# Kernel optimization log

Measured on AMD Instinct MI355X. Metric: run time of the kernel, lower is better.

Reference implementation:

```python
import jax, jax.numpy as jnp
import numpy as np

N = 100000   # nodes
E = 1600000  # edges (avg degree 16)
F_IN = 128
H = 128
C = 16


def setup_inputs() -> dict:
    key = jax.random.key(0)
    ks = jax.random.split(key, 13)
    s = 1.0 / np.sqrt(H)
    return {
        "x": jax.random.normal(ks[0], (N, F_IN), jnp.float32),
        "edge_index": jax.random.randint(ks[1], (2, E), 0, N, jnp.int32),
        "edge_weight": jax.random.uniform(ks[2], (E,), jnp.float32),
        "W1": jax.random.normal(ks[3], (F_IN, H), jnp.float32) * s,
        "b1": jnp.zeros((H,), jnp.float32),
        "W2": jax.random.normal(ks[4], (H, H), jnp.float32) * s,
        "b2": jnp.zeros((H,), jnp.float32),
        "Wg": jax.random.normal(ks[5], (H, H), jnp.float32) * s,
        "att_src": jax.random.normal(ks[6], (H,), jnp.float32) * s,
        "att_dst": jax.random.normal(ks[7], (H,), jnp.float32) * s,
        "bg": jnp.zeros((H,), jnp.float32),
        "Wc": jax.random.normal(ks[8], (H, C), jnp.float32) * s,
        "bc": jnp.zeros((C,), jnp.float32),
    }


def reference(x, edge_index, edge_weight, W1, b1, W2, b2, Wg, att_src, att_dst, bg, Wc, bc):
    n = x.shape[0]
    loop = jnp.arange(n, dtype=edge_index.dtype)
    src = jnp.concatenate([edge_index[0], loop])   # self loops (PyG default)
    dst = jnp.concatenate([edge_index[1], loop])
    ew = jnp.concatenate([edge_weight, jnp.ones((n,), x.dtype)])  # loop weight 1

    # GCN normalization: D^{-1/2} A D^{-1/2}, degree on dst with edge weights
    deg = jax.ops.segment_sum(ew, dst, num_segments=n)
    dinv = jnp.where(deg > 0, jax.lax.rsqrt(deg), 0.0)
    norm = dinv[src] * ew * dinv[dst]              # [E+N]

    def gcn(h, W, b):
        h = h @ W                                   # [N,H]
        agg = jax.ops.segment_sum(h[src] * norm[:, None], dst, num_segments=n)
        return agg + b

    h = jax.nn.relu(gcn(x, W1, b1))
    h = jax.nn.relu(gcn(h, W2, b2))                 # dropout inert in eval

    # GATConv, heads=1
    g = h @ Wg                                      # [N,H]
    a = jax.nn.leaky_relu((g @ att_src)[src] + (g @ att_dst)[dst], 0.2)
    amax = jax.ops.segment_max(a, dst, num_segments=n)
    ex = jnp.exp(a - amax[dst])
    denom = jax.ops.segment_sum(ex, dst, num_segments=n)
    alpha = ex / denom[dst]                         # edge softmax per dst
    out = jax.ops.segment_sum(g[src] * alpha[:, None], dst, num_segments=n) + bg
    out = jax.nn.relu(out)
    return out @ Wc + bc
```

## Files before the change

### kernel.cpp

```cpp
#include <hip/hip_runtime.h>
#include <hip/hip_fp16.h>

#define FIN 128
#define HD 128
#define COUT 16

#define SLOT_CAP 48
#define CS_BLOCKS 512
#define CB_SHIFT 9
#define CB_SIZE 512
#define CAP_B 10240
#define GMK_CELLS 64

typedef _Float16 half8 __attribute__((ext_vector_type(8)));
typedef float floatx4 __attribute__((ext_vector_type(4)));

__device__ __forceinline__ float lrelu02(float x) { return x > 0.f ? x : 0.2f * x; }

union U4H8 { uint4 q; __half2 h2[4]; };
union UQH8 { uint4 q; half8 h; _Float16 e[8]; };

__device__ __forceinline__ void h8f(const uint4 q, float* f) {
    U4H8 u; u.q = q;
    float2 a0 = __half22float2(u.h2[0]);
    float2 a1 = __half22float2(u.h2[1]);
    float2 a2 = __half22float2(u.h2[2]);
    float2 a3 = __half22float2(u.h2[3]);
    f[0] = a0.x; f[1] = a0.y; f[2] = a1.x; f[3] = a1.y;
    f[4] = a2.x; f[5] = a2.y; f[6] = a3.x; f[7] = a3.y;
}

__device__ __forceinline__ unsigned fkey(float f) {
    unsigned u = __float_as_uint(f);
    return (u & 0x80000000u) ? ~u : (u | 0x80000000u);
}
__device__ __forceinline__ float funkey(unsigned k) {
    return (k & 0x80000000u) ? __uint_as_float(k ^ 0x80000000u)
                             : __uint_as_float(~k);
}

__global__ void k_setup(const float* __restrict__ W1, const float* __restrict__ W2,
                        const float* __restrict__ Wg, __half* __restrict__ w1z,
                        __half* __restrict__ w2z, __half* __restrict__ wgz,
                        int* __restrict__ cur, unsigned* __restrict__ gmk) {
    int b = blockIdx.x;
    if (b < 24) {
        const float* W = (b < 8) ? W1 : (b < 16) ? W2 : Wg;
        __half* outp   = (b < 8) ? w1z : (b < 16) ? w2z : wgz;
        int t = (b & 7) * 256 + threadIdx.x;
        int lane = t & 63;
        int kc = (t >> 6) & 3;
        int nt = t >> 8;
        int kbase = kc * 32 + (lane >> 4) * 8;
        int col = nt * 16 + (lane & 15);
        UQH8 u;
#pragma unroll
        for (int j = 0; j < 8; j++)
            u.e[j] = (_Float16)W[(kbase + j) * 128 + col];
        ((uint4*)outp)[t] = u.q;
    } else {
        cur[threadIdx.x] = 0;
        for (int i = threadIdx.x; i < GMK_CELLS * 16; i += 256)
            gmk[i] = 0u;
    }
}

__device__ __forceinline__
void gemm_body_f32(int blk, const float* __restrict__ A, const __half* __restrict__ Wz,
                   __half* __restrict__ Out, int n) {
    int wave = threadIdx.x >> 6;
    int lane = threadIdx.x & 63;
    int m0 = blk * 64 + wave * 16;
    if (m0 >= n) return;
    int m = lane & 15;
    int quad = lane >> 4;

    half8 a[4];
#pragma unroll
    for (int kc = 0; kc < 4; kc++) {
        const float* p = &A[(size_t)(m0 + m) * 128 + kc * 32 + quad * 8];
        float4 f0 = *(const float4*)p;
        float4 f1 = *(const float4*)(p + 4);
        UQH8 u;
        u.e[0] = (_Float16)f0.x; u.e[1] = (_Float16)f0.y;
        u.e[2] = (_Float16)f0.z; u.e[3] = (_Float16)f0.w;
        u.e[4] = (_Float16)f1.x; u.e[5] = (_Float16)f1.y;
        u.e[6] = (_Float16)f1.z; u.e[7] = (_Float16)f1.w;
        a[kc] = u.h;
    }

    floatx4 acc[8];
#pragma unroll
    for (int nt = 0; nt < 8; nt++) acc[nt] = (floatx4){0.f, 0.f, 0.f, 0.f};

    const uint4* Wv = (const uint4*)Wz;
#pragma unroll
    for (int kc = 0; kc < 4; kc++) {
#pragma unroll
        for (int nt = 0; nt < 8; nt++) {
            UQH8 u;
            u.q = Wv[(nt * 4 + kc) * 64 + lane];
            acc[nt] = __builtin_amdgcn_mfma_f32_16x16x32_f16(a[kc], u.h, acc[nt], 0, 0, 0);
        }
    }
#pragma unroll
    for (int nt = 0; nt < 8; nt++) {
#pragma unroll
        for (int reg = 0; reg < 4; reg++) {
            Out[(size_t)(m0 + quad * 4 + reg) * 128 + nt * 16 + m] =
                __float2half(acc[nt][reg]);
        }
    }
}

__launch_bounds__(256)
__global__ void k_csc_gemm(const int* __restrict__ src, const int* __restrict__ dst,
                           const float* __restrict__ ew, int* __restrict__ cur,
                           int2* __restrict__ coarseBuf, int e,
                           const float* __restrict__ x, const __half* __restrict__ w1z,
                           __half* __restrict__ buf0, int n) {
    __shared__ int lcnt[256], lbase[256], lpos[256];
    if ((int)blockIdx.x < CS_BLOCKS) {
        int tid = threadIdx.x;
        lcnt[tid] = 0; lpos[tid] = 0;
        __syncthreads();
        int chunk = (e + CS_BLOCKS - 1) / CS_BLOCKS;
        int s0 = blockIdx.x * chunk;
        int s1 = min(s0 + chunk, e);
        for (int i = s0 + tid; i < s1; i += 256)
            atomicAdd(&lcnt[dst[i] >> CB_SHIFT], 1);
        __syncthreads();
        if (lcnt[tid] > 0) lbase[tid] = atomicAdd(&cur[tid], lcnt[tid]);
        __syncthreads();
        for (int i = s0 + tid; i < s1; i += 256) {
            int d = dst[i];
            int b = d >> CB_SHIFT;
            int pos = lbase[b] + atomicAdd(&lpos[b], 1);
            if (pos < CAP_B)
                coarseBuf[(size_t)b * CAP_B + pos] =
                    make_int2(((d & (CB_SIZE - 1)) << 17) | src[i], __float_as_int(ew[i]));
        }
    } else {
        gemm_body_f32(blockIdx.x - CS_BLOCKS, x, w1z, buf0, n);
    }
}

__launch_bounds__(512)
__global__ void k_fine(const int2* __restrict__ coarseBuf, const int* __restrict__ cur,
                       int2* __restrict__ slots, int* __restrict__ cnt,
                       float* __restrict__ dinv, int n) {
    __shared__ int lcnt[CB_SIZE];
    __shared__ float lsum[CB_SIZE];
    int b = blockIdx.x;
    int tid = threadIdx.x;
    if (tid < CB_SIZE) { lcnt[tid] = 0; lsum[tid] = 0.f; }
    __syncthreads();
    int ecnt = min(cur[b], CAP_B);
    size_t e0 = (size_t)b * CAP_B;
    for (int e = tid; e < ecnt; e += 512) {
        int2 it = coarseBuf[e0 + e];
        int dl = (it.x >> 17) & (CB_SIZE - 1);
        int srcn = it.x & 0x1FFFF;
        int pos = atomicAdd(&lcnt[dl], 1);
        atomicAdd(&lsum[dl], __int_as_float(it.y));
        if (pos < SLOT_CAP) {
            int node = (b << CB_SHIFT) + dl;
            slots[(size_t)node * SLOT_CAP + pos] = make_int2(srcn, it.y);
        }
    }
    __syncthreads();
    if (tid < CB_SIZE) {
        int node = (b << CB_SHIFT) + tid;
        if (node < n) {
            cnt[node] = min(lcnt[tid], SLOT_CAP);
            dinv[node] = rsqrtf(1.0f + lsum[tid]);
        }
    }
}

__device__ __forceinline__
void gather_body(int node, int lane, const int* __restrict__ cnt,
                 const int2* __restrict__ slots, const uint4* __restrict__ tv,
                 const float* __restrict__ dinv, const float* __restrict__ b,
                 float* __restrict__ fout) {
    float dd = dinv[node];
    float sw = dd * dd;
    float acc[8];
    {
        uint4 q = tv[(size_t)node * 16 + lane];
        float f[8]; h8f(q, f);
#pragma unroll
        for (int j = 0; j < 8; j++) acc[j] = f[j] * sw;
    }
    int r0 = (int)((size_t)node * SLOT_CAP);
    int r1 = r0 + cnt[node];
    int e = r0;
    for (; e + 8 <= r1; e += 8) {
        int2 c[8];
        float dv[8];
        uint4 v[8];
#pragma unroll
        for (int j = 0; j < 8; j++) c[j] = slots[e + j];
#pragma unroll
        for (int j = 0; j < 8; j++) dv[j] = dinv[c[j].x];
#pragma unroll
        for (int j = 0; j < 8; j++) v[j] = tv[(size_t)c[j].x * 16 + lane];
#pragma unroll
        for (int j = 0; j < 8; j++) {
            float w = dv[j] * __int_as_float(c[j].y) * dd;
            float f[8]; h8f(v[j], f);
#pragma unroll
            for (int k = 0; k < 8; k++) acc[k] = fmaf(f[k], w, acc[k]);
        }
    }
    for (; e + 2 <= r1; e += 2) {
        int2 c0 = slots[e], c1 = slots[e + 1];
        float dv0 = dinv[c0.x], dv1 = dinv[c1.x];
        uint4 v0 = tv[(size_t)c0.x * 16 + lane];
        uint4 v1 = tv[(size_t)c1.x * 16 + lane];
        float w0 = dv0 * __int_as_float(c0.y) * dd;
        float w1 = dv1 * __int_as_float(c1.y) * dd;
        float f0[8], f1[8]; h8f(v0, f0); h8f(v1, f1);
#pragma unroll
        for (int k = 0; k < 8; k++) acc[k] = fmaf(f0[k], w0, acc[k]);
#pragma unroll
        for (int k = 0; k < 8; k++) acc[k] = fmaf(f1[k], w1, acc[k]);
    }
    if (e < r1) {
        int2 c = slots[e];
        uint4 v = tv[(size_t)c.x * 16 + lane];
        float w = dinv[c.x] * __int_as_float(c.y) * dd;
        float f[8]; h8f(v, f);
#pragma unroll
        for (int k = 0; k < 8; k++) acc[k] = fmaf(f[k], w, acc[k]);
    }
    const float4* b4 = (const float4*)b;
    float4 bb0 = b4[lane * 2], bb1 = b4[lane * 2 + 1];
    fout[0] = fmaxf(acc[0] + bb0.x, 0.f);
    fout[1] = fmaxf(acc[1] + bb0.y, 0.f);
    fout[2] = fmaxf(acc[2] + bb0.z, 0.f);
    fout[3] = fmaxf(acc[3] + bb0.w, 0.f);
    fout[4] = fmaxf(acc[4] + bb1.x, 0.f);
    fout[5] = fmaxf(acc[5] + bb1.y, 0.f);
    fout[6] = fmaxf(acc[6] + bb1.z, 0.f);
    fout[7] = fmaxf(acc[7] + bb1.w, 0.f);
}

template <bool ATTN>
__launch_bounds__(256)
__global__ void k_gather_gemm(const int* __restrict__ cnt, const int2* __restrict__ slots,
                              const __half* __restrict__ t, const float* __restrict__ dinv,
                              const float* __restrict__ b, const __half* __restrict__ Wz,
                              __half* __restrict__ Out,
                              const float* __restrict__ attS, const float* __restrict__ attD,
                              float* __restrict__ as_, float* __restrict__ ad_,
                              unsigned* __restrict__ gmaxKey, int n) {
    __shared__ __half stage[16][136];
    __shared__ float redS[4][16], redD[4][16];
    int tid = threadIdx.x;
    int nl = tid >> 4;
    int lane16 = tid & 15;
    int node = blockIdx.x * 16 + nl;

    if (node < n) {
        float f[8];
        gather_body(node, lane16, cnt, slots, (const uint4*)t, dinv, b, f);
        UQH8 u;
#pragma unroll
        for (int j = 0; j < 8; j++) u.e[j] = (_Float16)f[j];
        *(uint4*)&stage[nl][lane16 * 8] = u.q;
    } else {
        UQH8 u;
#pragma unroll
        for (int j = 0; j < 8; j++) u.e[j] = (_Float16)0.f;
        *(uint4*)&stage[nl][lane16 * 8] = u.q;
    }
    __syncthreads();

    int wave = tid >> 6;
    int lane = tid & 63;
    int m = lane & 15;
    int quad = lane >> 4;
    int m0 = blockIdx.x * 16;

    half8 a[4];
#pragma unroll
    for (int kc = 0; kc < 4; kc++)
        a[kc] = *(const half8*)&stage[m][kc * 32 + quad * 8];

    floatx4 acc[2];
    acc[0] = (floatx4){0.f, 0.f, 0.f, 0.f};
    acc[1] = (floatx4){0.f, 0.f, 0.f, 0.f};
    const uint4* Wv = (const uint4*)Wz;
#pragma unroll
    for (int t2 = 0; t2 < 2; t2++) {
        int nt = wave * 2 + t2;
#pragma unroll
        for (int kc = 0; kc < 4; kc++) {
            UQH8 u;
            u.q = Wv[(nt * 4 + kc) * 64 + lane];
            acc[t2] = __builtin_amdgcn_mfma_f32_16x16x32_f16(a[kc], u.h, acc[t2], 0, 0, 0);
        }
    }
#pragma unroll
    for (int t2 = 0; t2 < 2; t2++) {
        int col = (wave * 2 + t2) * 16 + m;
#pragma unroll
        for (int reg = 0; reg < 4; reg++) {
            int row = m0 + quad * 4 + reg;
            if (row < n)
                Out[(size_t)row * 128 + col] = __float2half(acc[t2][reg]);
        }
    }

    if (ATTN) {
        float sv0 = attS[(wave * 2 + 0) * 16 + m], sv1 = attS[(wave * 2 + 1) * 16 + m];
        float dv0 = attD[(wave * 2 + 0) * 16 + m], dv1 = attD[(wave * 2 + 1) * 16 + m];
#pragma unroll
        for (int reg = 0; reg < 4; reg++) {
            float s = acc[0][reg] * sv0 + acc[1][reg] * sv1;
            float d = acc[0][reg] * dv0 + acc[1][reg] * dv1;
#pragma unroll
            for (int k = 8; k >= 1; k >>= 1) {
                s += __shfl_xor(s, k, 64);
                d += __shfl_xor(d, k, 64);
            }
            if (m == 0) {
                redS[wave][quad * 4 + reg] = s;
                redD[wave][quad * 4 + reg] = d;
            }
        }
        __syncthreads();
        if (tid < 16) {
            int nd = m0 + tid;
            unsigned key = 0u;
            if (nd < n) {
                float sv = redS[0][tid] + redS[1][tid] + redS[2][tid] + redS[3][tid];
                float dv = redD[0][tid] + redD[1][tid] + redD[2][tid] + redD[3][tid];
                as_[nd] = sv;
                ad_[nd] = dv;
                key = fkey(sv);
            }
#pragma unroll
            for (int k = 8; k >= 1; k >>= 1) {
                unsigned o = (unsigned)__shfl_xor((int)key, k, 64);
                key = key > o ? key : o;
            }
            if (tid == 0)
                atomicMax(&gmaxKey[(blockIdx.x & (GMK_CELLS - 1)) << 4], key);
        }
    }
}

__launch_bounds__(256)
__global__ void k_gat_final(const int* __restrict__ cnt, const int2* __restrict__ slots,
                            const __half* __restrict__ g, const float* __restrict__ as_,
                            const float* __restrict__ ad_,
                            const unsigned* __restrict__ gmaxKey,
                            const float* __restrict__ bg,
                            const float* __restrict__ Wc, const float* __restrict__ bc,
                            float* __restrict__ out, int n) {
    __shared__ float Wcs[128 * 16];
    __shared__ float bcs[16];
    __shared__ float stage[16][136];
    __shared__ float gmaxS;
    int tid = threadIdx.x;
    for (int i = tid; i < 128 * 16; i += 256) Wcs[i] = Wc[i];
    if (tid < 16) bcs[tid] = bc[tid];

    if (tid < 64) {
        unsigned k = gmaxKey[tid << 4];
#pragma unroll
        for (int d = 32; d >= 1; d >>= 1) {
            unsigned o = (unsigned)__shfl_xor((int)k, d, 64);
            k = k > o ? k : o;
        }
        if (tid == 0) gmaxS = funkey(k);
    }
    __syncthreads();
    float gmax = gmaxS;

    int idx = blockIdx.x * 256 + tid;
    int node = idx >> 4;
    int lane = idx & 15;
    int nl = tid >> 4;

    if (node < n) {
        int r0 = (int)((size_t)node * SLOT_CAP);
        int r1 = r0 + cnt[node];
        float ad_d = ad_[node];
        float c = lrelu02(gmax + ad_d);
        const uint4* gv = (const uint4*)g;
        float ex = __expf(lrelu02(as_[node] + ad_d) - c);
        float den = ex;
        float acc[8];
        {
            uint4 q = gv[(size_t)node * 16 + lane];
            float f[8]; h8f(q, f);
#pragma unroll
            for (int j = 0; j < 8; j++) acc[j] = ex * f[j];
        }
        int e = r0;
        for (; e + 8 <= r1; e += 8) {
            int s[8];
            uint4 u[8];
#pragma unroll
            for (int j = 0; j < 8; j++) s[j] = slots[e + j].x;
#pragma unroll
            for (int j = 0; j < 8; j++) u[j] = gv[(size_t)s[j] * 16 + lane];
#pragma unroll
            for (int j = 0; j < 8; j++) {
                float w = __expf(lrelu02(as_[s[j]] + ad_d) - c);
                den += w;
                float f[8]; h8f(u[j], f);
#pragma unroll
                for (int k = 0; k < 8; k++) acc[k] = fmaf(f[k], w, acc[k]);
            }
        }
        for (; e + 2 <= r1; e += 2) {
            int s0 = slots[e].x, s1 = slots[e + 1].x;
            uint4 u0 = gv[(size_t)s0 * 16 + lane];
            uint4 u1 = gv[(size_t)s1 * 16 + lane];
            float w0 = __expf(lrelu02(as_[s0] + ad_d) - c);
            float w1 = __expf(lrelu02(as_[s1] + ad_d) - c);
            den += w0 + w1;
            float f0[8], f1[8]; h8f(u0, f0); h8f(u1, f1);
#pragma unroll
            for (int k = 0; k < 8; k++) acc[k] = fmaf(f0[k], w0, acc[k]);
#pragma unroll
            for (int k = 0; k < 8; k++) acc[k] = fmaf(f1[k], w1, acc[k]);
        }
        if (e < r1) {
            int s = slots[e].x;
            uint4 u = gv[(size_t)s * 16 + lane];
            float w = __expf(lrelu02(as_[s] + ad_d) - c);
            den += w;
            float f[8]; h8f(u, f);
#pragma unroll
            for (int k = 0; k < 8; k++) acc[k] = fmaf(f[k], w, acc[k]);
        }
        float inv = 1.0f / den;
        const float4* bg4 = (const float4*)bg;
        float4 b0 = bg4[lane * 2], b1 = bg4[lane * 2 + 1];
        float* sp = &stage[nl][lane * 8];
        sp[0] = fmaxf(acc[0] * inv + b0.x, 0.f);
        sp[1] = fmaxf(acc[1] * inv + b0.y, 0.f);
        sp[2] = fmaxf(acc[2] * inv + b0.z, 0.f);
        sp[3] = fmaxf(acc[3] * inv + b0.w, 0.f);
        sp[4] = fmaxf(acc[4] * inv + b1.x, 0.f);
        sp[5] = fmaxf(acc[5] * inv + b1.y, 0.f);
        sp[6] = fmaxf(acc[6] * inv + b1.z, 0.f);
        sp[7] = fmaxf(acc[7] * inv + b1.w, 0.f);
    }
    __syncthreads();
    int nl2 = tid >> 4;
    int col = tid & 15;
    int onode = blockIdx.x * 16 + nl2;
    if (onode >= n) return;
    float accp = bcs[col];
    const float* sp = stage[nl2];
#pragma unroll 8
    for (int k = 0; k < 128; k++)
        accp = fmaf(sp[k], Wcs[k * 16 + col], accp);
    out[(size_t)onode * 16 + col] = accp;
}

extern "C" void kernel_launch(void* const* d_in, const int* in_sizes, int n_in,
                              void* d_out, int out_size, void* d_ws, size_t ws_size,
                              hipStream_t stream) {
    const float* x      = (const float*)d_in[0];
    const int*   eidx   = (const int*)d_in[1];
    const float* ew     = (const float*)d_in[2];
    const float* W1     = (const float*)d_in[3];
    const float* b1     = (const float*)d_in[4];
    const float* W2     = (const float*)d_in[5];
    const float* b2     = (const float*)d_in[6];
    const float* Wg     = (const float*)d_in[7];
    const float* attS   = (const float*)d_in[8];
    const float* attD   = (const float*)d_in[9];
    const float* bg     = (const float*)d_in[10];
    const float* Wc     = (const float*)d_in[11];
    const float* bc     = (const float*)d_in[12];

    const int N = in_sizes[0] / FIN;
    const int E = in_sizes[2];
    const int* src = eidx;
    const int* dst = eidx + E;
    const int NB = (N + CB_SIZE - 1) >> CB_SHIFT;

    char* base = (char*)d_ws;
    size_t off = 0;
    auto carve = [&](size_t bytes) {
        char* q = base + off;
        off = (off + bytes + 255) & ~(size_t)255;
        return (void*)q;
    };
    int*    cnt       = (int*)carve((size_t)N * 4);
    int*    cur       = (int*)carve(256 * 4);
    unsigned* gmk     = (unsigned*)carve((size_t)GMK_CELLS * 16 * 4);
    int2*   coarseBuf = (int2*)carve((size_t)NB * CAP_B * 8);
    int2*   slots     = (int2*)carve((size_t)N * SLOT_CAP * 8);
    float*  dinv      = (float*)carve((size_t)N * 4);
    float*  as_       = (float*)carve((size_t)N * 4);
    float*  ad_       = (float*)carve((size_t)N * 4);
    __half* w1z       = (__half*)carve((size_t)128 * 128 * 2);
    __half* w2z       = (__half*)carve((size_t)128 * 128 * 2);
    __half* wgz       = (__half*)carve((size_t)128 * 128 * 2);
    __half* buf0      = (__half*)carve((size_t)N * 128 * 2);
    __half* buf1      = (__half*)carve((size_t)N * 128 * 2);

    const int B = 256;
    dim3 blk(B);
    int fusedGrid = (N + 15) / 16;
    int gemmGrid = (N + 63) / 64;

    k_setup<<<25, blk, 0, stream>>>(W1, W2, Wg, w1z, w2z, wgz, cur, gmk);
    k_csc_gemm<<<CS_BLOCKS + gemmGrid, blk, 0, stream>>>(src, dst, ew, cur, coarseBuf, E,
                                                         x, w1z, buf0, N);
    k_fine<<<NB, dim3(512), 0, stream>>>(coarseBuf, cur, slots, cnt, dinv, N);

    k_gather_gemm<false><<<fusedGrid, blk, 0, stream>>>(cnt, slots, buf0, dinv, b1, w2z,
                                                        buf1, nullptr, nullptr,
                                                        nullptr, nullptr, nullptr, N);
    k_gather_gemm<true><<<fusedGrid, blk, 0, stream>>>(cnt, slots, buf1, dinv, b2, wgz,
                                                       buf0, attS, attD, as_, ad_, gmk, N);
    k_gat_final<<<fusedGrid, blk, 0, stream>>>(cnt, slots, buf0, as_, ad_, gmk, bg,
                                               Wc, bc, (float*)d_out, N);
}
```

Measured before the change: 418.5 us.

## Sort nodes by in-degree into a permutation to balance gather workloads

Builds a per-degree histogram in the fine CSC pass, prefix-sums it, and scatters node ids into a degree-sorted permutation. The three gather kernels then process nodes in that order, so the 16 nodes sharing a block have similar edge counts and lanes diverge less. Outputs are written back through the permutation. The final GAT loop also prefetches attention scores into registers before the feature loads. This adds two small kernels and an indirection, and loses locality between neighbouring node ids in output writes.

```diff
diff --git a/kernel.cpp b/kernel.cpp
--- a/kernel.cpp
+++ b/kernel.cpp
@@ -11,6 +11,7 @@
 #define CB_SIZE 512
 #define CAP_B 10240
 #define GMK_CELLS 64
+#define NBINS 49
 
 typedef _Float16 half8 __attribute__((ext_vector_type(8)));
 typedef float floatx4 __attribute__((ext_vector_type(4)));
@@ -42,7 +43,8 @@
 __global__ void k_setup(const float* __restrict__ W1, const float* __restrict__ W2,
                         const float* __restrict__ Wg, __half* __restrict__ w1z,
                         __half* __restrict__ w2z, __half* __restrict__ wgz,
-                        int* __restrict__ cur, unsigned* __restrict__ gmk) {
+                        int* __restrict__ cur, unsigned* __restrict__ gmk,
+                        int* __restrict__ hist) {
     int b = blockIdx.x;
     if (b < 24) {
         const float* W = (b < 8) ? W1 : (b < 16) ? W2 : Wg;
@@ -60,6 +62,7 @@
         ((uint4*)outp)[t] = u.q;
     } else {
         cur[threadIdx.x] = 0;
+        if (threadIdx.x < 64) hist[threadIdx.x] = 0;
         for (int i = threadIdx.x; i < GMK_CELLS * 16; i += 256)
             gmk[i] = 0u;
     }
@@ -148,12 +151,15 @@
 __launch_bounds__(512)
 __global__ void k_fine(const int2* __restrict__ coarseBuf, const int* __restrict__ cur,
                        int2* __restrict__ slots, int* __restrict__ cnt,
-                       float* __restrict__ dinv, int n) {
+                       float* __restrict__ dinv, int* __restrict__ hist, int n) {
     __shared__ int lcnt[CB_SIZE];
     __shared__ float lsum[CB_SIZE];
+    __shared__ int lhist[NBINS];
     int b = blockIdx.x;
     int tid = threadIdx.x;
     if (tid < CB_SIZE) { lcnt[tid] = 0; lsum[tid] = 0.f; }
+    if (tid >= CB_SIZE && tid - CB_SIZE < NBINS) lhist[tid - CB_SIZE] = 0;
+    if (tid < NBINS && CB_SIZE >= 512) lhist[tid] = 0;
     __syncthreads();
     int ecnt = min(cur[b], CAP_B);
     size_t e0 = (size_t)b * CAP_B;
@@ -172,9 +178,39 @@
     if (tid < CB_SIZE) {
         int node = (b << CB_SHIFT) + tid;
         if (node < n) {
-            cnt[node] = min(lcnt[tid], SLOT_CAP);
+            int c = min(lcnt[tid], SLOT_CAP);
+            cnt[node] = c;
             dinv[node] = rsqrtf(1.0f + lsum[tid]);
-        }
+            atomicAdd(&lhist[c], 1);
+        }
+    }
+    __syncthreads();
+    if (tid < NBINS && lhist[tid] > 0) atomicAdd(&hist[tid], lhist[tid]);
+}
+
+__global__ void k_prefix(const int* __restrict__ hist, int* __restrict__ binCur) {
+    if (threadIdx.x == 0) {
+        int acc = 0;
+        for (int c = 0; c < NBINS; c++) { binCur[c] = acc; acc += hist[c]; }
+    }
+}
+
+__launch_bounds__(512)
+__global__ void k_permscatter(const int* __restrict__ cnt, int* __restrict__ binCur,
+                              int* __restrict__ perm, int n) {
+    __shared__ int lh[NBINS], lb[NBINS], lp[NBINS];
+    int tid = threadIdx.x;
+    if (tid < NBINS) { lh[tid] = 0; lp[tid] = 0; }
+    __syncthreads();
+    int node = blockIdx.x * 512 + tid;
+    int c = -1;
+    if (node < n) { c = cnt[node]; atomicAdd(&lh[c], 1); }
+    __syncthreads();
+    if (tid < NBINS && lh[tid] > 0) lb[tid] = atomicAdd(&binCur[tid], lh[tid]);
+    __syncthreads();
+    if (node < n) {
+        int pos = lb[c] + atomicAdd(&lp[c], 1);
+        perm[pos] = node;
     }
 }
 
@@ -251,7 +287,7 @@
 __global__ void k_gather_gemm(const int* __restrict__ cnt, const int2* __restrict__ slots,
                               const __half* __restrict__ t, const float* __restrict__ dinv,
                               const float* __restrict__ b, const __half* __restrict__ Wz,
-                              __half* __restrict__ Out,
+                              __half* __restrict__ Out, const int* __restrict__ perm,
                               const float* __restrict__ attS, const float* __restrict__ attD,
                               float* __restrict__ as_, float* __restrict__ ad_,
                               unsigned* __restrict__ gmaxKey, int n) {
@@ -260,9 +296,10 @@
     int tid = threadIdx.x;
     int nl = tid >> 4;
     int lane16 = tid & 15;
-    int node = blockIdx.x * 16 + nl;
-
-    if (node < n) {
+    int idx16 = blockIdx.x * 16 + nl;
+    int node = (idx16 < n) ? perm[idx16] : -1;
+
+    if (node >= 0) {
         float f[8];
         gather_body(node, lane16, cnt, slots, (const uint4*)t, dinv, b, f);
         UQH8 u;
@@ -303,13 +340,15 @@
         }
     }
 #pragma unroll
-    for (int t2 = 0; t2 < 2; t2++) {
-        int col = (wave * 2 + t2) * 16 + m;
-#pragma unroll
-        for (int reg = 0; reg < 4; reg++) {
-            int row = m0 + quad * 4 + reg;
-            if (row < n)
-                Out[(size_t)row * 128 + col] = __float2half(acc[t2][reg]);
+    for (int reg = 0; reg < 4; reg++) {
+        int row = m0 + quad * 4 + reg;
+        if (row < n) {
+            int prow = perm[row];
+#pragma unroll
+            for (int t2 = 0; t2 < 2; t2++) {
+                int col = (wave * 2 + t2) * 16 + m;
+                Out[(size_t)prow * 128 + col] = __float2half(acc[t2][reg]);
+            }
         }
     }
 
@@ -337,8 +376,9 @@
             if (nd < n) {
                 float sv = redS[0][tid] + redS[1][tid] + redS[2][tid] + redS[3][tid];
                 float dv = redD[0][tid] + redD[1][tid] + redD[2][tid] + redD[3][tid];
-                as_[nd] = sv;
-                ad_[nd] = dv;
+                int pn = perm[nd];
+                as_[pn] = sv;
+                ad_[pn] = dv;
                 key = fkey(sv);
             }
 #pragma unroll
@@ -357,6 +397,7 @@
                             const __half* __restrict__ g, const float* __restrict__ as_,
                             const float* __restrict__ ad_,
                             const unsigned* __restrict__ gmaxKey,
+                            const int* __restrict__ perm,
                             const float* __restrict__ bg,
                             const float* __restrict__ Wc, const float* __restrict__ bc,
                             float* __restrict__ out, int n) {
@@ -381,11 +422,12 @@
     float gmax = gmaxS;
 
     int idx = blockIdx.x * 256 + tid;
-    int node = idx >> 4;
+    int lidx = idx >> 4;
+    int node = (lidx < n) ? perm[lidx] : -1;
     int lane = idx & 15;
     int nl = tid >> 4;
 
-    if (node < n) {
+    if (node >= 0) {
         int r0 = (int)((size_t)node * SLOT_CAP);
         int r1 = r0 + cnt[node];
         float ad_d = ad_[node];
@@ -403,14 +445,17 @@
         int e = r0;
         for (; e + 8 <= r1; e += 8) {
             int s[8];
+            float av[8];
             uint4 u[8];
 #pragma unroll
             for (int j = 0; j < 8; j++) s[j] = slots[e + j].x;
 #pragma unroll
+            for (int j = 0; j < 8; j++) av[j] = as_[s[j]];
+#pragma unroll
             for (int j = 0; j < 8; j++) u[j] = gv[(size_t)s[j] * 16 + lane];
 #pragma unroll
             for (int j = 0; j < 8; j++) {
-                float w = __expf(lrelu02(as_[s[j]] + ad_d) - c);
+                float w = __expf(lrelu02(av[j] + ad_d) - c);
                 den += w;
                 float f[8]; h8f(u[j], f);
 #pragma unroll
@@ -455,8 +500,9 @@
     __syncthreads();
     int nl2 = tid >> 4;
     int col = tid & 15;
-    int onode = blockIdx.x * 16 + nl2;
-    if (onode >= n) return;
+    int oidx = blockIdx.x * 16 + nl2;
+    if (oidx >= n) return;
+    int onode = perm[oidx];
     float accp = bcs[col];
     const float* sp = stage[nl2];
 #pragma unroll 8
@@ -498,6 +544,9 @@
     int*    cnt       = (int*)carve((size_t)N * 4);
     int*    cur       = (int*)carve(256 * 4);
     unsigned* gmk     = (unsigned*)carve((size_t)GMK_CELLS * 16 * 4);
+    int*    hist      = (int*)carve(64 * 4);
+    int*    binCur    = (int*)carve(64 * 4);
+    int*    perm      = (int*)carve((size_t)N * 4);
     int2*   coarseBuf = (int2*)carve((size_t)NB * CAP_B * 8);
     int2*   slots     = (int2*)carve((size_t)N * SLOT_CAP * 8);
     float*  dinv      = (float*)carve((size_t)N * 4);
@@ -514,16 +563,19 @@
     int fusedGrid = (N + 15) / 16;
     int gemmGrid = (N + 63) / 64;
 
-    k_setup<<<25, blk, 0, stream>>>(W1, W2, Wg, w1z, w2z, wgz, cur, gmk);
+    k_setup<<<25, blk, 0, stream>>>(W1, W2, Wg, w1z, w2z, wgz, cur, gmk, hist);
     k_csc_gemm<<<CS_BLOCKS + gemmGrid, blk, 0, stream>>>(src, dst, ew, cur, coarseBuf, E,
                                                          x, w1z, buf0, N);
-    k_fine<<<NB, dim3(512), 0, stream>>>(coarseBuf, cur, slots, cnt, dinv, N);
+    k_fine<<<NB, dim3(512), 0, stream>>>(coarseBuf, cur, slots, cnt, dinv, hist, N);
+    k_prefix<<<1, dim3(64), 0, stream>>>(hist, binCur);
+    k_permscatter<<<NB, dim3(512), 0, stream>>>(cnt, binCur, perm, N);
 
     k_gather_gemm<false><<<fusedGrid, blk, 0, stream>>>(cnt, slots, buf0, dinv, b1, w2z,
-                                                        buf1, nullptr, nullptr,
+                                                        buf1, perm, nullptr, nullptr,
                                                         nullptr, nullptr, nullptr, N);
     k_gather_gemm<true><<<fusedGrid, blk, 0, stream>>>(cnt, slots, buf1, dinv, b2, wgz,
-                                                       buf0, attS, attD, as_, ad_, gmk, N);
-    k_gat_final<<<fusedGrid, blk, 0, stream>>>(cnt, slots, buf0, as_, ad_, gmk, bg,
+                                                       buf0, perm, attS, attD, as_, ad_,
+                                                       gmk, N);
+    k_gat_final<<<fusedGrid, blk, 0, stream>>>(cnt, slots, buf0, as_, ad_, gmk, perm, bg,
                                                Wc, bc, (float*)d_out, N);
 }
```

New measurement: 414.4 us. About the same (-1.0%).
